# Optimization experiments

Hardware: AMD Instinct MI355X
Metric: run time of the kernel (lower is better)

The kernel has to match this reference:

```python
import jax, jax.numpy as jnp
import numpy as np
from jax import lax

K = 3          # spline order
G = 5          # grid intervals
R0, R1 = -4.0, 4.0  # grid_range
IN, HID, OUT = 32, 128, 16
BATCH, SEQ = 256, 512


def make_grid(n_in):
    # extended knot vector: G+2K+1 knots per input, uniform spacing h
    h = (R1 - R0) / G
    knots = R0 + h * jnp.arange(-K, G + K + 1, dtype=jnp.float32)  # [G+2K+1]
    return jnp.broadcast_to(knots, (n_in, G + 2 * K + 1))


def b_splines(x, grid):
    # Cox-de Boor recursion. x: [B, n], grid: [n, G+2K+1] -> basis [B, n, G+K]
    xg = x[..., None]
    B = ((xg >= grid[:, :-1]) & (xg < grid[:, 1:])).astype(x.dtype)
    for d in range(1, K + 1):
        B = ((xg - grid[:, :-(d + 1)]) / (grid[:, d:-1] - grid[:, :-(d + 1)]) * B[..., :-1]
             + (grid[:, d + 1:] - xg) / (grid[:, d + 1:] - grid[:, 1:-d]) * B[..., 1:])
    return B


def kan_layer(x, coef, scale_base, scale_sp, grid):
    # y[b,o] = sum_i scale_base[i,o]*silu(x[b,i]) + scale_sp[i,o]*spline_io(x[b,i])
    base = jax.nn.silu(x)                               # [B, n_in]
    Bsp = b_splines(x, grid)                            # [B, n_in, G+K]
    spline = jnp.einsum('bik,iok->bio', Bsp, coef)      # [B, n_in, n_out]
    return (jnp.einsum('bi,io->bo', base, scale_base)
            + jnp.einsum('bio,io->bo', spline, scale_sp))


def setup_inputs() -> dict:
    key = jax.random.key(0)
    ks = jax.random.split(key, 7)
    x = jax.random.normal(ks[0], (BATCH, SEQ, IN), dtype=jnp.float32)
    coef1 = jax.random.normal(ks[1], (IN + HID, HID, G + K), dtype=jnp.float32) * 0.1
    sb1 = jax.random.normal(ks[2], (IN + HID, HID), dtype=jnp.float32) * 0.05
    sp1 = jax.random.normal(ks[3], (IN + HID, HID), dtype=jnp.float32) * 0.05
    coef2 = jax.random.normal(ks[4], (HID, OUT, G + K), dtype=jnp.float32) * 0.1
    sb2 = jax.random.normal(ks[5], (HID, OUT), dtype=jnp.float32) * 0.05
    sp2 = jax.random.normal(ks[6], (HID, OUT), dtype=jnp.float32) * 0.05
    return {"x": x, "coef1": coef1, "sb1": sb1, "sp1": sp1,
            "coef2": coef2, "sb2": sb2, "sp2": sp2}


def reference(x, coef1, sb1, sp1, coef2, sb2, sp2):
    grid1 = make_grid(IN + HID)
    grid2 = make_grid(HID)

    def step(h, x_t):
        combined = jnp.concatenate([x_t, h], axis=1)        # [B, IN+HID]
        h_new = kan_layer(combined, coef1, sb1, sp1, grid1)  # [B, HID]
        out_t = kan_layer(h_new, coef2, sb2, sp2, grid2)     # [B, OUT]
        return h_new, out_t

    h0 = jnp.zeros((x.shape[0], HID), dtype=x.dtype)
    _, outs = lax.scan(step, h0, jnp.swapaxes(x, 0, 1))  # outs: [T, B, OUT]
    # original stacks all timestep outputs then returns outputs[:, -1, :]
    return outs[-1]
```

## Files before the change

kernel.cpp:

```cpp
#include <hip/hip_runtime.h>
#include <hip/hip_bf16.h>

#define NIN 32
#define NHID 128
#define NOUT 16
#define NIN1 160
#define SEQT 512
#define NB 256
#define SEGI 40

#if defined(__has_builtin)
#if __has_builtin(__builtin_amdgcn_fdot2_f32_bf16)
#define HAVE_DOT2BF 1
#endif
#endif
#ifndef HAVE_DOT2BF
#define HAVE_DOT2BF 0
#endif

__device__ __forceinline__ unsigned int f2bfbits(float f) {
    unsigned int u = __float_as_uint(f);
    return (u + 0x7fffu + ((u >> 16) & 1u)) >> 16;
}
__device__ __forceinline__ unsigned int packbf(float lo, float hi) {
    return f2bfbits(lo) | (f2bfbits(hi) << 16);
}

#if HAVE_DOT2BF
typedef __bf16 bf16x2 __attribute__((ext_vector_type(2)));
__device__ __forceinline__ float dot2w(unsigned int a, unsigned int b, float c) {
    return __builtin_amdgcn_fdot2_f32_bf16(__builtin_bit_cast(bf16x2, a),
                                           __builtin_bit_cast(bf16x2, b), c, false);
}
#else
__device__ __forceinline__ float dot2w(unsigned int a, unsigned int b, float c) {
    float alo = __uint_as_float(a << 16), ahi = __uint_as_float(a & 0xffff0000u);
    float blo = __uint_as_float(b << 16), bhi = __uint_as_float(b & 0xffff0000u);
    return __builtin_fmaf(ahi, bhi, __builtin_fmaf(alo, blo, c));
}
#endif

__device__ __forceinline__ void spline_feat(float c, float* out4, int* jst) {
    const float t0 = -8.8f, hh = 1.6f;
    int m0 = (int)floorf((c - t0) / hh);
    bool valid = (m0 >= 0) && (m0 <= 10);
    float v0 = 1.f, v1 = 0.f, v2 = 0.f, v3 = 0.f;
    #pragma unroll
    for (int d = 1; d <= 3; ++d) {
        float inv = 1.f / (d * hh);
        float nv[4];
        float pv[4] = {v0, v1, v2, v3};
        #pragma unroll
        for (int r = 3; r >= 0; --r) {
            if (r > d) { nv[r] = 0.f; continue; }
            int m = m0 - d + r;
            float tm = t0 + hh * (float)m;
            float left  = (r >= 1) ? pv[r-1] : 0.f;
            float right = (r <= d-1) ? pv[r] : 0.f;
            nv[r] = ((c - tm) * left + (tm + hh * (float)(d+1) - c) * right) * inv;
        }
        v0 = nv[0]; v1 = nv[1]; v2 = nv[2]; v3 = nv[3];
    }
    float v[4] = {v0, v1, v2, v3};
    int jb = m0 - 3;
    int js = jb < 0 ? 0 : (jb > 4 ? 4 : jb);
    int sh = js - jb;
    #pragma unroll
    for (int r = 0; r < 4; ++r) {
        int rs = r + sh;
        out4[r] = (valid && rs >= 0 && rs <= 3) ? v[rs] : 0.f;
    }
    *jst = js;
}

__device__ __forceinline__ float fsilu(float c) {
    return c * __builtin_amdgcn_rcpf(1.f + __expf(-c));
}

#define R20(X) X(0) X(1) X(2) X(3) X(4) X(5) X(6) X(7) X(8) X(9) \
               X(10) X(11) X(12) X(13) X(14) X(15) X(16) X(17) X(18) X(19)

__attribute__((amdgpu_waves_per_eu(2, 2)))
__global__ void __launch_bounds__(512)
kan_seq(const float* __restrict__ x,
        const float* __restrict__ coef1,
        const float* __restrict__ sb1,
        const float* __restrict__ sp1,
        const float* __restrict__ coef2,
        const float* __restrict__ sb2,
        const float* __restrict__ sp2,
        float* __restrict__ out)
{
    __shared__ __align__(16) unsigned int Fb[NIN1][4];
    __shared__ float Fsil[NIN1];
    __shared__ float red[4][NHID];
    __shared__ float Hf[NHID][9];

    const int tid  = threadIdx.x;
    const int b    = blockIdx.x;
    const int o    = tid & 127;
    const int seg  = tid >> 7;
    const int i0   = seg * SEGI;
    const int lane = tid & 63;

#define DECLP(p) uint4 wA##p, wB##p; unsigned int sbp##p;
    R20(DECLP)
#undef DECLP

#define INITP(p) { \
    const int iA = i0 + 2 * (p), iB = i0 + 2 * (p) + 1; \
    const float4* ca = (const float4*)(coef1 + (size_t)(iA * NHID + o) * 8); \
    const float4* cb = (const float4*)(coef1 + (size_t)(iB * NHID + o) * 8); \
    float spA = sp1[iA * NHID + o], spB = sp1[iB * NHID + o]; \
    float4 a0 = ca[0], a1 = ca[1], b0v = cb[0], b1v = cb[1]; \
    wA##p = make_uint4(packbf(spA * a0.x, spA * a0.y), packbf(spA * a0.z, spA * a0.w), \
                       packbf(spA * a1.x, spA * a1.y), packbf(spA * a1.z, spA * a1.w)); \
    wB##p = make_uint4(packbf(spB * b0v.x, spB * b0v.y), packbf(spB * b0v.z, spB * b0v.w), \
                       packbf(spB * b1v.x, spB * b1v.y), packbf(spB * b1v.z, spB * b1v.w)); \
    sbp##p = packbf(sb1[iA * NHID + o], sb1[iB * NHID + o]); }
    R20(INITP)
#undef INITP

    ((float*)red)[tid] = 0.f;
    float xv = (tid < NIN) ? x[(size_t)b * SEQT * NIN + tid] : 0.f;
    __syncthreads();

    for (int t = 0; t < SEQT; ++t) {
        if (tid < NIN1) {
            float c;
            if (tid < NIN) c = xv;
            else {
                int hi = tid - NIN;
                c = red[0][hi] + red[1][hi] + red[2][hi] + red[3][hi];
            }
            float sil = fsilu(c);
            float b4[4]; int js;
            spline_feat(c, b4, &js);
            float e[8];
            #pragma unroll
            for (int k = 0; k < 8; ++k) {
                int d = k - js;
                e[k] = (d >= 0 && d < 4) ? b4[d] : 0.f;
            }
            uint4 pk;
            pk.x = packbf(e[0], e[1]); pk.y = packbf(e[2], e[3]);
            pk.z = packbf(e[4], e[5]); pk.w = packbf(e[6], e[7]);
            *(uint4*)&Fb[tid][0] = pk;
            Fsil[tid] = sil;
        }
        if (tid < NIN) {
            int tn = (t + 1 < SEQT) ? (t + 1) : t;
            xv = x[((size_t)b * SEQT + tn) * NIN + tid];
        }
        __syncthreads();

        float vsil = Fsil[i0 + (lane < SEGI ? lane : 0)];
        float ac0 = 0.f, ac1 = 0.f, ac2 = 0.f, ac3 = 0.f;
#define DOTP(p) { \
        float sb_lo = __uint_as_float(sbp##p << 16); \
        float sb_hi = __uint_as_float(sbp##p & 0xffff0000u); \
        float slA = __int_as_float(__builtin_amdgcn_readlane(__float_as_int(vsil), 2 * (p))); \
        float slB = __int_as_float(__builtin_amdgcn_readlane(__float_as_int(vsil), 2 * (p) + 1)); \
        uint4 bA = *(const uint4*)&Fb[i0 + 2 * (p)][0]; \
        uint4 bB = *(const uint4*)&Fb[i0 + 2 * (p) + 1][0]; \
        ac0 = __builtin_fmaf(slA, sb_lo, ac0); \
        ac0 = dot2w(bA.x, wA##p.x, ac0); ac1 = dot2w(bA.y, wA##p.y, ac1); \
        ac2 = dot2w(bA.z, wA##p.z, ac2); ac3 = dot2w(bA.w, wA##p.w, ac3); \
        ac1 = __builtin_fmaf(slB, sb_hi, ac1); \
        ac0 = dot2w(bB.x, wB##p.x, ac0); ac1 = dot2w(bB.y, wB##p.y, ac1); \
        ac2 = dot2w(bB.z, wB##p.z, ac2); ac3 = dot2w(bB.w, wB##p.w, ac3); }
        R20(DOTP)
#undef DOTP
        red[seg][o] = (ac0 + ac1) + (ac2 + ac3);
        __syncthreads();
    }

    if (tid < NHID) {
        float c = red[0][tid] + red[1][tid] + red[2][tid] + red[3][tid];
        float sil = fsilu(c);
        float b4[4]; int js;
        spline_feat(c, b4, &js);
        #pragma unroll
        for (int k = 0; k < 8; ++k) {
            int d = k - js;
            Hf[tid][k] = (d >= 0 && d < 4) ? b4[d] : 0.f;
        }
        Hf[tid][8] = sil;
    }
    __syncthreads();
    if (tid < 128) {
        int o2 = tid & 15, isg = tid >> 4;
        float acc = 0.f;
        for (int q = 0; q < 16; ++q) {
            int i = isg * 16 + q;
            const float* c2 = coef2 + (size_t)(i * NOUT + o2) * 8;
            float s = 0.f;
            #pragma unroll
            for (int k = 0; k < 8; ++k) s += Hf[i][k] * c2[k];
            acc += Hf[i][8] * sb2[i * NOUT + o2] + sp2[i * NOUT + o2] * s;
        }
        ((float*)red)[isg * 16 + o2] = acc;
    }
    __syncthreads();
    if (tid < NOUT) {
        float a = 0.f;
        #pragma unroll
        for (int g = 0; g < 8; ++g) a += ((float*)red)[g * 16 + tid];
        out[(size_t)b * NOUT + tid] = a;
    }
}

extern "C" void kernel_launch(void* const* d_in, const int* in_sizes, int n_in,
                              void* d_out, int out_size, void* d_ws, size_t ws_size,
                              hipStream_t stream) {
    kan_seq<<<NB, 512, 0, stream>>>(
        (const float*)d_in[0], (const float*)d_in[1], (const float*)d_in[2],
        (const float*)d_in[3], (const float*)d_in[4], (const float*)d_in[5],
        (const float*)d_in[6], (float*)d_out);
}
```

Measured before the change: 1.051 ms.

## Use closed-form uniform cubic B-spline basis and software-prefetch LDS features

Replaces the Cox-de Boor recursion in spline_feat with the closed-form uniform cubic B-spline polynomials in the fractional knot position. This removes divisions and the per-degree loop from the serial per-timestep feature stage. It also double-buffers the LDS loads of the packed basis features in the dot-product loop so each pair is loaded one iteration ahead. Risks are small numerical differences near knot boundaries and higher register pressure from the prefetch under the 2-waves-per-EU limit.

Result: faster. 983.3 us (-6.5%).

```diff
diff --git a/kernel.cpp b/kernel.cpp
--- a/kernel.cpp
+++ b/kernel.cpp
@@ -41,26 +41,20 @@
 #endif
 
 __device__ __forceinline__ void spline_feat(float c, float* out4, int* jst) {
-    const float t0 = -8.8f, hh = 1.6f;
-    int m0 = (int)floorf((c - t0) / hh);
+    const float t0 = -8.8f, inv_h = 0.625f;
+    float u  = (c - t0) * inv_h;
+    float uf = floorf(u);
+    int   m0 = (int)uf;
     bool valid = (m0 >= 0) && (m0 <= 10);
-    float v0 = 1.f, v1 = 0.f, v2 = 0.f, v3 = 0.f;
-    #pragma unroll
-    for (int d = 1; d <= 3; ++d) {
-        float inv = 1.f / (d * hh);
-        float nv[4];
-        float pv[4] = {v0, v1, v2, v3};
-        #pragma unroll
-        for (int r = 3; r >= 0; --r) {
-            if (r > d) { nv[r] = 0.f; continue; }
-            int m = m0 - d + r;
-            float tm = t0 + hh * (float)m;
-            float left  = (r >= 1) ? pv[r-1] : 0.f;
-            float right = (r <= d-1) ? pv[r] : 0.f;
-            nv[r] = ((c - tm) * left + (tm + hh * (float)(d+1) - c) * right) * inv;
-        }
-        v0 = nv[0]; v1 = nv[1]; v2 = nv[2]; v3 = nv[3];
-    }
+    float f   = u - uf;
+    float omf = 1.0f - f;
+    float f2 = f * f,     f3 = f2 * f;
+    float omf3 = omf * omf * omf;
+    const float c6 = 0.16666667f;
+    float v0 = omf3 * c6;
+    float v1 = __builtin_fmaf(3.0f, f3, __builtin_fmaf(-6.0f, f2, 4.0f)) * c6;
+    float v2 = __builtin_fmaf(-3.0f, f3, __builtin_fmaf(3.0f, f + f2, 1.0f)) * c6;
+    float v3 = f3 * c6;
     float v[4] = {v0, v1, v2, v3};
     int jb = m0 - 3;
     int js = jb < 0 ? 0 : (jb > 4 ? 4 : jb);
@@ -155,14 +149,19 @@
         __syncthreads();
 
         float vsil = Fsil[i0 + (lane < SEGI ? lane : 0)];
+        uint4 pfA = *(const uint4*)&Fb[i0][0];
+        uint4 pfB = *(const uint4*)&Fb[i0 + 1][0];
         float ac0 = 0.f, ac1 = 0.f, ac2 = 0.f, ac3 = 0.f;
 #define DOTP(p) { \
+        uint4 bA = pfA, bB = pfB; \
+        if ((p) < SEGI / 2 - 1) { \
+            pfA = *(const uint4*)&Fb[i0 + 2 * (p) + 2][0]; \
+            pfB = *(const uint4*)&Fb[i0 + 2 * (p) + 3][0]; \
+        } \
         float sb_lo = __uint_as_float(sbp##p << 16); \
         float sb_hi = __uint_as_float(sbp##p & 0xffff0000u); \
         float slA = __int_as_float(__builtin_amdgcn_readlane(__float_as_int(vsil), 2 * (p))); \
         float slB = __int_as_float(__builtin_amdgcn_readlane(__float_as_int(vsil), 2 * (p) + 1)); \
-        uint4 bA = *(const uint4*)&Fb[i0 + 2 * (p)][0]; \
-        uint4 bB = *(const uint4*)&Fb[i0 + 2 * (p) + 1][0]; \
         ac0 = __builtin_fmaf(slA, sb_lo, ac0); \
         ac0 = dot2w(bA.x, wA##p.x, ac0); ac1 = dot2w(bA.y, wA##p.y, ac1); \
         ac2 = dot2w(bA.z, wA##p.z, ac2); ac3 = dot2w(bA.w, wA##p.w, ac3); \
```
